# Kernel tuning notes

Measured on AMD Instinct MI355X. Metric: run time of the kernel, lower is better.

## Reference

```python
import jax, jax.numpy as jnp
import numpy as np
from jax import lax

B, C, H, W = 64, 64, 56, 56
E, TOPK = 8, 2
DN = ('NCHW', 'OIHW', 'NCHW')


def setup_inputs() -> dict:
    key = jax.random.key(0)
    ks = jax.random.split(key, 9)
    s = 0.05
    return {
        'x': jax.random.normal(ks[0], (B, C, H, W), jnp.float32),
        'gate_w': jax.random.normal(ks[1], (E, C), jnp.float32) * s,
        'gate_b': jnp.zeros((E,), jnp.float32),
        'conv1_w': jax.random.normal(ks[2], (E, C, C, 3, 3), jnp.float32) * s,
        'bn1_s': jnp.ones((E, C), jnp.float32),
        'bn1_b': jnp.zeros((E, C), jnp.float32),
        'conv2_w': jax.random.normal(ks[3], (E, C, C, 3, 3), jnp.float32) * s,
        'bn2_s': jnp.ones((E, C), jnp.float32),
        'bn2_b': jnp.zeros((E, C), jnp.float32),
    }


def _conv3x3(x, w):
    return lax.conv_general_dilated(x, w, (1, 1), ((1, 1), (1, 1)), dimension_numbers=DN)


def _bn(y, scale, bias):
    # eval-mode BatchNorm with running_mean=0, running_var=1 -> per-channel affine
    return y * scale[None, :, None, None] + bias[None, :, None, None]


def _basic_block(x, w1, s1, b1, w2, s2, b2):
    # standard ResNet BasicBlock, stride=1, identity downsample
    out = jax.nn.relu(_bn(_conv3x3(x, w1), s1, b1))
    out = _bn(_conv3x3(out, w2), s2, b2)
    return jax.nn.relu(out + x)


def reference(x, gate_w, gate_b, conv1_w, bn1_s, bn1_b, conv2_w, bn2_s, bn2_b):
    # gate: global average pool over HW -> linear -> top-k softmax weights [B, E]
    pooled = jnp.mean(x, axis=(2, 3))                       # [B, C]
    logits = pooled @ gate_w.T + gate_b                      # [B, E]
    top_vals, top_idx = lax.top_k(logits, TOPK)              # [B, K]
    top_w = jax.nn.softmax(top_vals, axis=-1)                # [B, K]
    dense_w = jnp.zeros((x.shape[0], E), x.dtype).at[
        jnp.arange(x.shape[0])[:, None], top_idx].set(top_w)  # [B, E]

    # run all experts (dense reference for the sparse dispatch/combine)
    ex_out = jax.vmap(lambda w1, s1, b1, w2, s2, b2: _basic_block(x, w1, s1, b1, w2, s2, b2))(
        conv1_w, bn1_s, bn1_b, conv2_w, bn2_s, bn2_b)        # [E, B, C, H, W]
    out = jnp.einsum('be,ebchw->bchw', dense_w, ex_out)
    return out, dense_w
```

## Files before the change

kernel.cpp:

```cpp
#include <hip/hip_runtime.h>


#define BATCH 64
#define CH    64
#define HW_   3136
#define IMG_  (CH*HW_)
#define PLANE (HW_*16)
#define NE    8
#define JOBS  128
#define PWSZ  36864
#define NTILE 13
#define BD    6
#define CGRID (NTILE*2*BATCH)

typedef unsigned short u16;
typedef __attribute__((ext_vector_type(8))) short short8_t;
typedef __attribute__((ext_vector_type(16))) float floatx16;

__device__ u16   g_xb[(size_t)BATCH * IMG_];
__device__ u16   g_h[(size_t)JOBS * IMG_];
__device__ u16   g_pw1[NE * PWSZ];
__device__ u16   g_pw2[NE * PWSZ];
__device__ int   g_eid[JOBS];
__device__ float g_wgt[JOBS];
__device__ float g_pool[49 * BATCH * CH];

__device__ __forceinline__ u16 f2b(float f) {
    unsigned v; __builtin_memcpy(&v, &f, 4);
    return (u16)((v + 0x7FFFu + ((v >> 16) & 1u)) >> 16);
}

__global__ __launch_bounds__(256) void pack_kernel(
    const float* __restrict__ w1, const float* __restrict__ s1,
    const float* __restrict__ w2, const float* __restrict__ s2)
{
    int idx = blockIdx.x * 256 + threadIdx.x;
    int conv = idx / 294912;
    int i2 = idx - conv * 294912;
    int e = i2 / PWSZ;   int r = i2 - e * PWSZ;
    int s36 = r >> 10;   int r2 = r & 1023;
    int mt  = r2 >> 9;   int r3 = r2 & 511;
    int h   = r3 >> 8;   int r4 = r3 & 255;
    int m   = r4 >> 3;   int j  = r4 & 7;
    int tap = s36 >> 2;
    int ci  = ((s36 & 3) << 4) | (h << 3) | j;
    int M   = mt*32 + m;
    const float* w  = conv ? w2 : w1;
    const float* sc = conv ? s2 : s1;
    float v = w[((e*64 + M)*64 + ci)*9 + tap] * sc[e*64 + M];
    (conv ? g_pw2 : g_pw1)[i2] = f2b(v);
}

__global__ __launch_bounds__(256) void xconv_kernel(const float* __restrict__ x)
{
    __shared__ u16 T[64*66];
    int b = blockIdx.y;
    int pos0 = blockIdx.x * 64;
    int tid = threadIdx.x;
    int pin = tid & 63;
    int c0 = tid >> 6;
    const float* xb = x + (size_t)b*IMG_ + pos0 + pin;
    #pragma unroll
    for (int i = 0; i < 16; i++) {
        int ch = c0*16 + i;
        T[pin*66 + ch] = f2b(xb[ch*HW_]);
    }
    __syncthreads();
    u16* ob = g_xb + (size_t)b*IMG_ + (size_t)pos0*16;
    #pragma unroll
    for (int i = 0; i < 16; i++) {
        int j = tid + i*256;
        int kq  = j >> 10;
        int pos = (j >> 4) & 63;
        int c16 = j & 15;
        ob[(size_t)kq*PLANE + pos*16 + c16] = T[pos*66 + kq*16 + c16];
    }
    if (tid < 64) {
        float s = 0.f;
        const float* xc = x + (size_t)b*IMG_ + tid*HW_ + pos0;
        #pragma unroll 4
        for (int p = 0; p < 64; p++) s += xc[p];
        g_pool[blockIdx.x*(BATCH*CH) + b*64 + tid] = s;
    }
}

__global__ __launch_bounds__(64) void gate_fin_kernel(
    const float* __restrict__ gw, const float* __restrict__ gb,
    float* __restrict__ dw_out)
{
    __shared__ float pooled[CH];
    __shared__ float logits[NE];
    int b = blockIdx.x, t = threadIdx.x;
    float s = 0.f;
    #pragma unroll
    for (int i = 0; i < 49; i++) s += g_pool[i*(BATCH*CH) + b*64 + t];
    pooled[t] = s * (1.f/3136.f);
    __syncthreads();
    if (t < NE) {
        float l = gb[t];
        for (int c = 0; c < CH; c++) l += pooled[c] * gw[t*CH + c];
        logits[t] = l;
    }
    __syncthreads();
    if (t == 0) {
        int i1 = 0; float v1 = logits[0];
        for (int e = 1; e < NE; e++) if (logits[e] > v1) { v1 = logits[e]; i1 = e; }
        int i2 = -1; float v2 = -3.4e38f;
        for (int e = 0; e < NE; e++) if (e != i1 && logits[e] > v2) { v2 = logits[e]; i2 = e; }
        float eb = __expf(v2 - v1);
        float wa = 1.f / (1.f + eb), wb = eb / (1.f + eb);
        for (int e = 0; e < NE; e++) dw_out[b*NE + e] = 0.f;
        dw_out[b*NE + i1] = wa;
        dw_out[b*NE + i2] = wb;
        g_eid[2*b] = i1; g_eid[2*b+1] = i2;
        g_wgt[2*b] = wa; g_wgt[2*b+1] = wb;
    }
}

__device__ __forceinline__ short8_t loadB32(
    const u16* __restrict__ in, int gn, int y, int xc, int tap, int kq)
{
    int dy = tap/3 - 1, dxk = tap - (tap/3)*3 - 1;
    int p = gn + dy*56 + dxk;
    bool vld = ((unsigned)(y + dy) < 56u) && ((unsigned)(xc + dxk) < 56u);
    int pc = p < 0 ? 0 : (p > 3135 ? 3135 : p);
    short8_t t = *(const short8_t*)(in + (size_t)kq*PLANE + pc*16);
    const short8_t zero = {};
    return vld ? t : zero;
}

__device__ __forceinline__ void stageA(
    u16* AL, const u16* __restrict__ pw0, const u16* __restrict__ pw1,
    int mt, int tid)
{
    short8_t st[9];
    #pragma unroll
    for (int i = 0; i < 9; i++) {
        int u = i*512 + tid;
        int es = u >= 2304;
        int r = u - (es ? 2304 : 0);
        int s36 = r >> 6;
        int c = r & 63;
        st[i] = *(const short8_t*)((es ? pw1 : pw0) + s36*1024 + mt*512 + c*8);
    }
    #pragma unroll
    for (int i = 0; i < 9; i++) {
        int u = i*512 + tid;
        int es = u >= 2304;
        int r = u - (es ? 2304 : 0);
        int s36 = r >> 6;
        int c = r & 63;
        *(short8_t*)(AL + (s36*2 + es)*512 + c*8) = st[i];
    }
}

__global__ __launch_bounds__(512, 4) void conv1_kernel(const float* __restrict__ b1)
{
    __shared__ u16 AL[36864];
    int wg = blockIdx.x;
    int L  = (wg & 7) * (CGRID/8) + (wg >> 3);
    int b  = L / 26;
    int r  = L - b*26;
    int tile = r >> 1;
    int mt   = r & 1;
    int e0 = g_eid[2*b], e1 = g_eid[2*b+1];
    int tid = threadIdx.x;
    int lane = tid & 63, w = tid >> 6;
    int es = w & 1, pg = w >> 1;
    int l31 = lane & 31, h = lane >> 5;
    int gn0 = tile*256 + pg*64 + l31;
    int gn1 = gn0 + 32;
    int y0 = gn0/56, xc0 = gn0 - y0*56;
    int y1 = gn1/56, xc1 = gn1 - y1*56;
    int e = es ? e1 : e0;
    const u16* in  = g_xb + (size_t)b*IMG_ + h*8;
    const u16* pw0 = g_pw1 + e0*PWSZ;
    const u16* pw1 = g_pw1 + e1*PWSZ;
    int aOff = es*512 + h*256 + l31*8;

    floatx16 accA = {}, accB = {};
    short8_t B0[BD], B1[BD];
    #pragma unroll
    for (int s = 0; s < BD; s++) {
        B0[s] = loadB32(in, gn0, y0, xc0, s >> 2, s & 3);
        B1[s] = loadB32(in, gn1, y1, xc1, s >> 2, s & 3);
    }
    stageA(AL, pw0, pw1, mt, tid);
    __syncthreads();

    short8_t Ar[3];
    #pragma unroll
    for (int i = 0; i < 3; i++)
        Ar[i] = *(const short8_t*)(AL + i*1024 + aOff);

    #pragma unroll
    for (int s = 0; s < 36; s++) {
        short8_t bb0 = B0[s % BD];
        short8_t bb1 = B1[s % BD];
        int sp = s + BD;
        if (sp < 36) {
            B0[s % BD] = loadB32(in, gn0, y0, xc0, sp >> 2, sp & 3);
            B1[s % BD] = loadB32(in, gn1, y1, xc1, sp >> 2, sp & 3);
        }
        short8_t a = Ar[s % 3];
        if (s + 3 < 36)
            Ar[s % 3] = *(const short8_t*)(AL + (s+3)*1024 + aOff);
        accA = __builtin_amdgcn_mfma_f32_32x32x16_bf16(a, bb0, accA, 0, 0, 0);
        accB = __builtin_amdgcn_mfma_f32_32x32x16_bf16(a, bb1, accB, 0, 0, 0);
    }

    u16* hb = g_h + (size_t)(2*b + es)*IMG_;
    #pragma unroll
    for (int f = 0; f < 2; f++) {
        int gn = f ? gn1 : gn0;
        if (gn < HW_) {
            #pragma unroll
            for (int rg = 0; rg < 4; rg++) {
                union { u16 u[4]; uint2 v; } t;
                #pragma unroll
                for (int rr = 0; rr < 4; rr++) {
                    int m = rg*8 + h*4 + rr;
                    float v = (f ? accB : accA)[rg*4 + rr] + b1[e*64 + mt*32 + m];
                    t.u[rr] = f2b(fmaxf(v, 0.f));
                }
                int kq = mt*2 + (rg >> 1);
                *(uint2*)(hb + (size_t)kq*PLANE + (size_t)gn*16 + (rg & 1)*8 + h*4) = t.v;
            }
        }
    }
}

__global__ __launch_bounds__(512, 4) void conv2_kernel(
    const float* __restrict__ x, const float* __restrict__ b2,
    float* __restrict__ out)
{
    __shared__ u16 AL[36864];
    int wg = blockIdx.x;
    int L  = (wg & 7) * (CGRID/8) + (wg >> 3);
    int b  = L / 26;
    int r  = L - b*26;
    int tile = (NTILE-1) - (r >> 1);
    int mt   = r & 1;
    int e0 = g_eid[2*b], e1 = g_eid[2*b+1];
    int tid = threadIdx.x;
    int lane = tid & 63, w = tid >> 6;
    int es = w & 1, pg = w >> 1;
    int l31 = lane & 31, h = lane >> 5;
    int gn0 = tile*256 + pg*64 + l31;
    int gn1 = gn0 + 32;
    int y0 = gn0/56, xc0 = gn0 - y0*56;
    int y1 = gn1/56, xc1 = gn1 - y1*56;
    int e = es ? e1 : e0;
    float wgt = g_wgt[2*b + es];
    const u16* in  = g_h + (size_t)(2*b + es)*IMG_ + h*8;
    const u16* pw0 = g_pw2 + e0*PWSZ;
    const u16* pw1 = g_pw2 + e1*PWSZ;
    int aOff = es*512 + h*256 + l31*8;

    floatx16 accA = {}, accB = {};
    short8_t B0[BD], B1[BD];
    #pragma unroll
    for (int s = 0; s < BD; s++) {
        B0[s] = loadB32(in, gn0, y0, xc0, s >> 2, s & 3);
        B1[s] = loadB32(in, gn1, y1, xc1, s >> 2, s & 3);
    }
    stageA(AL, pw0, pw1, mt, tid);
    __syncthreads();

    short8_t Ar[3];
    #pragma unroll
    for (int i = 0; i < 3; i++)
        Ar[i] = *(const short8_t*)(AL + i*1024 + aOff);

    #pragma unroll
    for (int s = 0; s < 36; s++) {
        short8_t bb0 = B0[s % BD];
        short8_t bb1 = B1[s % BD];
        int sp = s + BD;
        if (sp < 36) {
            B0[s % BD] = loadB32(in, gn0, y0, xc0, sp >> 2, sp & 3);
            B1[s % BD] = loadB32(in, gn1, y1, xc1, sp >> 2, sp & 3);
        }
        short8_t a = Ar[s % 3];
        if (s + 3 < 36)
            Ar[s % 3] = *(const short8_t*)(AL + (s+3)*1024 + aOff);
        accA = __builtin_amdgcn_mfma_f32_32x32x16_bf16(a, bb0, accA, 0, 0, 0);
        accB = __builtin_amdgcn_mfma_f32_32x32x16_bf16(a, bb1, accB, 0, 0, 0);
    }

    __syncthreads();
    float* P = (float*)AL;
    const float* xb = x + (size_t)b*IMG_ + (size_t)(mt*32)*HW_;
    if (es == 0) {
        #pragma unroll
        for (int f = 0; f < 2; f++) {
            int gn = f ? gn1 : gn0;
            if (gn < HW_) {
                #pragma unroll
                for (int rg = 0; rg < 4; rg++)
                    #pragma unroll
                    for (int rr = 0; rr < 4; rr++) {
                        int m = rg*8 + h*4 + rr;
                        float v = (f ? accB : accA)[rg*4 + rr] + b2[e*64 + mt*32 + m]
                                  + xb[(size_t)m*HW_ + gn];
                        P[((pg*2 + f)*32 + m)*32 + l31] = wgt * fmaxf(v, 0.f);
                    }
            }
        }
    }
    __syncthreads();
    if (es == 1) {
        float* ob = out + (size_t)b*IMG_ + (size_t)(mt*32)*HW_;
        #pragma unroll
        for (int f = 0; f < 2; f++) {
            int gn = f ? gn1 : gn0;
            if (gn < HW_) {
                #pragma unroll
                for (int rg = 0; rg < 4; rg++)
                    #pragma unroll
                    for (int rr = 0; rr < 4; rr++) {
                        int m = rg*8 + h*4 + rr;
                        float v = (f ? accB : accA)[rg*4 + rr] + b2[e*64 + mt*32 + m]
                                  + xb[(size_t)m*HW_ + gn];
                        ob[(size_t)m*HW_ + gn] = wgt * fmaxf(v, 0.f)
                                                 + P[((pg*2 + f)*32 + m)*32 + l31];
                    }
            }
        }
    }
}

extern "C" void kernel_launch(void* const* d_in, const int* in_sizes, int n_in,
                              void* d_out, int out_size, void* d_ws, size_t ws_size,
                              hipStream_t stream) {
    const float* x   = (const float*)d_in[0];
    const float* gw  = (const float*)d_in[1];
    const float* gb  = (const float*)d_in[2];
    const float* w1  = (const float*)d_in[3];
    const float* s1  = (const float*)d_in[4];
    const float* b1  = (const float*)d_in[5];
    const float* w2  = (const float*)d_in[6];
    const float* s2  = (const float*)d_in[7];
    const float* b2  = (const float*)d_in[8];
    float* out = (float*)d_out;
    float* dw  = out + (size_t)BATCH * IMG_;

    (void)d_ws; (void)ws_size;

    hipLaunchKernelGGL(pack_kernel, dim3(2304), dim3(256), 0, stream, w1, s1, w2, s2);
    hipLaunchKernelGGL(xconv_kernel, dim3(49, BATCH), dim3(256), 0, stream, x);
    hipLaunchKernelGGL(gate_fin_kernel, dim3(BATCH), dim3(64), 0, stream, gw, gb, dw);
    hipLaunchKernelGGL(conv1_kernel, dim3(CGRID), dim3(512), 0, stream, b1);
    hipLaunchKernelGGL(conv2_kernel, dim3(CGRID), dim3(512), 0, stream, x, b2, out);
}
```

Before: 241.6 us.

## Fuse pack, layout conversion and gating into one prep kernel; precompute B-load offsets

Merges weight packing, the activation bf16/layout conversion and the gate computation into a single prep kernel. Per-batch pooling is accumulated with atomics, and a last-block ticket counter performs the top-k gating, which removes two launches and the 49-slice partial pool buffer. Separately, the conv kernels now precompute per-tap byte offsets once. Out-of-image taps point to a zero-padded tail region appended to the buffers, so the per-load clamp and select are gone. The risks are the atomic float pooling changing summation order and relying on the padding staying zero.

```diff
diff --git a/kernel.cpp b/kernel.cpp
--- a/kernel.cpp
+++ b/kernel.cpp
@@ -17,46 +17,55 @@
 typedef __attribute__((ext_vector_type(8))) short short8_t;
 typedef __attribute__((ext_vector_type(16))) float floatx16;
 
-__device__ u16   g_xb[(size_t)BATCH * IMG_];
-__device__ u16   g_h[(size_t)JOBS * IMG_];
+__device__ u16   g_xb[(size_t)BATCH*IMG_ + 4*PLANE];
+__device__ u16   g_h[(size_t)JOBS*IMG_ + 4*PLANE];
 __device__ u16   g_pw1[NE * PWSZ];
 __device__ u16   g_pw2[NE * PWSZ];
 __device__ int   g_eid[JOBS];
 __device__ float g_wgt[JOBS];
-__device__ float g_pool[49 * BATCH * CH];
+__device__ float g_pool[BATCH * CH];
+__device__ unsigned g_tick[BATCH];
 
 __device__ __forceinline__ u16 f2b(float f) {
     unsigned v; __builtin_memcpy(&v, &f, 4);
     return (u16)((v + 0x7FFFu + ((v >> 16) & 1u)) >> 16);
 }
 
-__global__ __launch_bounds__(256) void pack_kernel(
+__global__ __launch_bounds__(256) void prep_kernel(
+    const float* __restrict__ x,
     const float* __restrict__ w1, const float* __restrict__ s1,
-    const float* __restrict__ w2, const float* __restrict__ s2)
-{
-    int idx = blockIdx.x * 256 + threadIdx.x;
-    int conv = idx / 294912;
-    int i2 = idx - conv * 294912;
-    int e = i2 / PWSZ;   int r = i2 - e * PWSZ;
-    int s36 = r >> 10;   int r2 = r & 1023;
-    int mt  = r2 >> 9;   int r3 = r2 & 511;
-    int h   = r3 >> 8;   int r4 = r3 & 255;
-    int m   = r4 >> 3;   int j  = r4 & 7;
-    int tap = s36 >> 2;
-    int ci  = ((s36 & 3) << 4) | (h << 3) | j;
-    int M   = mt*32 + m;
-    const float* w  = conv ? w2 : w1;
-    const float* sc = conv ? s2 : s1;
-    float v = w[((e*64 + M)*64 + ci)*9 + tap] * sc[e*64 + M];
-    (conv ? g_pw2 : g_pw1)[i2] = f2b(v);
-}
-
-__global__ __launch_bounds__(256) void xconv_kernel(const float* __restrict__ x)
-{
+    const float* __restrict__ w2, const float* __restrict__ s2,
+    const float* __restrict__ gw, const float* __restrict__ gb,
+    float* __restrict__ dw_out)
+{
+    int bid = blockIdx.x;
+    int tid = threadIdx.x;
+    if (bid < 2304) {
+        int idx = bid * 256 + tid;
+        int conv = idx / 294912;
+        int i2 = idx - conv * 294912;
+        int e = i2 / PWSZ;   int r = i2 - e * PWSZ;
+        int s36 = r >> 10;   int r2 = r & 1023;
+        int mt  = r2 >> 9;   int r3 = r2 & 511;
+        int h   = r3 >> 8;   int r4 = r3 & 255;
+        int m   = r4 >> 3;   int j  = r4 & 7;
+        int tap = s36 >> 2;
+        int ci  = ((s36 & 3) << 4) | (h << 3) | j;
+        int M   = mt*32 + m;
+        const float* w  = conv ? w2 : w1;
+        const float* sc = conv ? s2 : s1;
+        float v = w[((e*64 + M)*64 + ci)*9 + tap] * sc[e*64 + M];
+        (conv ? g_pw2 : g_pw1)[i2] = f2b(v);
+        return;
+    }
     __shared__ u16 T[64*66];
-    int b = blockIdx.y;
-    int pos0 = blockIdx.x * 64;
-    int tid = threadIdx.x;
+    __shared__ float pooled[CH];
+    __shared__ float logits[NE];
+    __shared__ int last;
+    int xid = bid - 2304;
+    int b = xid / 49;
+    int tile = xid - b*49;
+    int pos0 = tile * 64;
     int pin = tid & 63;
     int c0 = tid >> 6;
     const float* xb = x + (size_t)b*IMG_ + pos0 + pin;
@@ -80,29 +89,29 @@
         const float* xc = x + (size_t)b*IMG_ + tid*HW_ + pos0;
         #pragma unroll 4
         for (int p = 0; p < 64; p++) s += xc[p];
-        g_pool[blockIdx.x*(BATCH*CH) + b*64 + tid] = s;
-    }
-}
-
-__global__ __launch_bounds__(64) void gate_fin_kernel(
-    const float* __restrict__ gw, const float* __restrict__ gb,
-    float* __restrict__ dw_out)
-{
-    __shared__ float pooled[CH];
-    __shared__ float logits[NE];
-    int b = blockIdx.x, t = threadIdx.x;
-    float s = 0.f;
-    #pragma unroll
-    for (int i = 0; i < 49; i++) s += g_pool[i*(BATCH*CH) + b*64 + t];
-    pooled[t] = s * (1.f/3136.f);
-    __syncthreads();
-    if (t < NE) {
-        float l = gb[t];
-        for (int c = 0; c < CH; c++) l += pooled[c] * gw[t*CH + c];
-        logits[t] = l;
-    }
-    __syncthreads();
-    if (t == 0) {
+        atomicAdd(&g_pool[b*64 + tid], s);
+    }
+    __syncthreads();
+    __threadfence();
+    if (tid == 0) {
+        unsigned o = atomicAdd(&g_tick[b], 1u);
+        last = (o == 48);
+        if (o == 48) g_tick[b] = 0;
+    }
+    __syncthreads();
+    if (!last) return;
+    if (tid < 64) {
+        float v = atomicExch(&g_pool[b*64 + tid], 0.f);
+        pooled[tid] = v * (1.f/3136.f);
+    }
+    __syncthreads();
+    if (tid < NE) {
+        float l = gb[tid];
+        for (int c = 0; c < CH; c++) l += pooled[c] * gw[tid*CH + c];
+        logits[tid] = l;
+    }
+    __syncthreads();
+    if (tid == 0) {
         int i1 = 0; float v1 = logits[0];
         for (int e = 1; e < NE; e++) if (logits[e] > v1) { v1 = logits[e]; i1 = e; }
         int i2 = -1; float v2 = -3.4e38f;
@@ -117,18 +126,6 @@
     }
 }
 
-__device__ __forceinline__ short8_t loadB32(
-    const u16* __restrict__ in, int gn, int y, int xc, int tap, int kq)
-{
-    int dy = tap/3 - 1, dxk = tap - (tap/3)*3 - 1;
-    int p = gn + dy*56 + dxk;
-    bool vld = ((unsigned)(y + dy) < 56u) && ((unsigned)(xc + dxk) < 56u);
-    int pc = p < 0 ? 0 : (p > 3135 ? 3135 : p);
-    short8_t t = *(const short8_t*)(in + (size_t)kq*PLANE + pc*16);
-    const short8_t zero = {};
-    return vld ? t : zero;
-}
-
 __device__ __forceinline__ void stageA(
     u16* AL, const u16* __restrict__ pw0, const u16* __restrict__ pw1,
     int mt, int tid)
@@ -153,6 +150,19 @@
         *(short8_t*)(AL + (s36*2 + es)*512 + c*8) = st[i];
     }
 }
+
+__device__ __forceinline__ void mkOffs(
+    unsigned* off, int gn, int y, int xc, int h, unsigned zoff)
+{
+    #pragma unroll
+    for (int tap = 0; tap < 9; tap++) {
+        int dy = tap/3 - 1, dx = tap - (tap/3)*3 - 1;
+        int p = gn + dy*56 + dx;
+        bool vld = ((unsigned)(y + dy) < 56u) && ((unsigned)(xc + dx) < 56u);
+        off[tap] = vld ? (unsigned)(p*32 + h*16) : zoff;
+    }
+}
+#define LOADB(base, off, kq) (*(const short8_t*)((base) + (off) + (unsigned)((kq)*PLANE*2)))
 
 __global__ __launch_bounds__(512, 4) void conv1_kernel(const float* __restrict__ b1)
 {
@@ -173,17 +183,22 @@
     int y0 = gn0/56, xc0 = gn0 - y0*56;
     int y1 = gn1/56, xc1 = gn1 - y1*56;
     int e = es ? e1 : e0;
-    const u16* in  = g_xb + (size_t)b*IMG_ + h*8;
+    const char* base = (const char*)(g_xb + (size_t)b*IMG_);
+    unsigned zoff = (unsigned)((size_t)(BATCH - b)*IMG_*2);
     const u16* pw0 = g_pw1 + e0*PWSZ;
     const u16* pw1 = g_pw1 + e1*PWSZ;
     int aOff = es*512 + h*256 + l31*8;
 
+    unsigned off0[9], off1[9];
+    mkOffs(off0, gn0, y0, xc0, h, zoff);
+    mkOffs(off1, gn1, y1, xc1, h, zoff);
+
     floatx16 accA = {}, accB = {};
     short8_t B0[BD], B1[BD];
     #pragma unroll
     for (int s = 0; s < BD; s++) {
-        B0[s] = loadB32(in, gn0, y0, xc0, s >> 2, s & 3);
-        B1[s] = loadB32(in, gn1, y1, xc1, s >> 2, s & 3);
+        B0[s] = LOADB(base, off0[s >> 2], s & 3);
+        B1[s] = LOADB(base, off1[s >> 2], s & 3);
     }
     stageA(AL, pw0, pw1, mt, tid);
     __syncthreads();
@@ -199,8 +214,8 @@
         short8_t bb1 = B1[s % BD];
         int sp = s + BD;
         if (sp < 36) {
-            B0[s % BD] = loadB32(in, gn0, y0, xc0, sp >> 2, sp & 3);
-            B1[s % BD] = loadB32(in, gn1, y1, xc1, sp >> 2, sp & 3);
+            B0[s % BD] = LOADB(base, off0[sp >> 2], sp & 3);
+            B1[s % BD] = LOADB(base, off1[sp >> 2], sp & 3);
         }
         short8_t a = Ar[s % 3];
         if (s + 3 < 36)
@@ -252,17 +267,22 @@
     int y1 = gn1/56, xc1 = gn1 - y1*56;
     int e = es ? e1 : e0;
     float wgt = g_wgt[2*b + es];
-    const u16* in  = g_h + (size_t)(2*b + es)*IMG_ + h*8;
+    const char* base = (const char*)(g_h + (size_t)(2*b + es)*IMG_);
+    unsigned zoff = (unsigned)((size_t)(JOBS - (2*b + es))*IMG_*2);
     const u16* pw0 = g_pw2 + e0*PWSZ;
     const u16* pw1 = g_pw2 + e1*PWSZ;
     int aOff = es*512 + h*256 + l31*8;
 
+    unsigned off0[9], off1[9];
+    mkOffs(off0, gn0, y0, xc0, h, zoff);
+    mkOffs(off1, gn1, y1, xc1, h, zoff);
+
     floatx16 accA = {}, accB = {};
     short8_t B0[BD], B1[BD];
     #pragma unroll
     for (int s = 0; s < BD; s++) {
-        B0[s] = loadB32(in, gn0, y0, xc0, s >> 2, s & 3);
-        B1[s] = loadB32(in, gn1, y1, xc1, s >> 2, s & 3);
+        B0[s] = LOADB(base, off0[s >> 2], s & 3);
+        B1[s] = LOADB(base, off1[s >> 2], s & 3);
     }
     stageA(AL, pw0, pw1, mt, tid);
     __syncthreads();
@@ -278,8 +298,8 @@
         short8_t bb1 = B1[s % BD];
         int sp = s + BD;
         if (sp < 36) {
-            B0[s % BD] = loadB32(in, gn0, y0, xc0, sp >> 2, sp & 3);
-            B1[s % BD] = loadB32(in, gn1, y1, xc1, sp >> 2, sp & 3);
+            B0[s % BD] = LOADB(base, off0[sp >> 2], sp & 3);
+            B1[s % BD] = LOADB(base, off1[sp >> 2], sp & 3);
         }
         short8_t a = Ar[s % 3];
         if (s + 3 < 36)
@@ -347,9 +367,8 @@
 
     (void)d_ws; (void)ws_size;
 
-    hipLaunchKernelGGL(pack_kernel, dim3(2304), dim3(256), 0, stream, w1, s1, w2, s2);
-    hipLaunchKernelGGL(xconv_kernel, dim3(49, BATCH), dim3(256), 0, stream, x);
-    hipLaunchKernelGGL(gate_fin_kernel, dim3(BATCH), dim3(64), 0, stream, gw, gb, dw);
+    hipLaunchKernelGGL(prep_kernel, dim3(2304 + 3136), dim3(256), 0, stream,
+                       x, w1, s1, w2, s2, gw, gb, dw);
     hipLaunchKernelGGL(conv1_kernel, dim3(CGRID), dim3(512), 0, stream, b1);
     hipLaunchKernelGGL(conv2_kernel, dim3(CGRID), dim3(512), 0, stream, x, b2, out);
 }
```

Result: slower. 546.0 us (+126.0%).
